# Performance work log

Hardware: AMD Instinct MI355X
Metric: run time of the kernel (lower is better)

Reference implementation:

```python
import jax, jax.numpy as jnp
import numpy as np


def setup_inputs() -> dict:
    key = jax.random.key(0)
    k1, k2, k3, k4, k5 = jax.random.split(key, 5)
    B, Di, Dh = 16384, 1024, 1024
    stdv = 1.0 / np.sqrt(Dh)
    return {
        "X": jax.random.normal(k1, (B, Di), dtype=jnp.float32),
        "h0": jax.random.normal(k2, (B, Dh), dtype=jnp.float32),
        "c0": jax.random.normal(k3, (B, Dh), dtype=jnp.float32),
        "U": jax.random.uniform(k4, (Di, 4 * Dh), dtype=jnp.float32, minval=-stdv, maxval=stdv),
        "W": jax.random.uniform(k5, (4 * Dh, Dh), dtype=jnp.float32, minval=-stdv, maxval=stdv),
    }


def reference(X, h0, c0, U, W):
    # Single-step LSTM cell: gates = X @ U + h0 @ W^T, split into i/f/g/o.
    Dh = h0.shape[-1]
    XU = X @ U                      # (B, 4*Dh)
    gates = XU + h0 @ W.T           # (B, 4*Dh)
    i, f, g, o = jnp.split(gates, 4, axis=-1)
    i = jax.nn.sigmoid(i)
    f = jax.nn.sigmoid(f)
    g = jnp.tanh(g)
    o = jax.nn.sigmoid(o)
    c = f * c0 + i * g              # (B, Dh)
    h = o * jnp.tanh(c)             # (B, Dh)
    return (h, c)
```

## Files before the change

kernel.cpp:

```cpp
#include <hip/hip_runtime.h>
#include <hip/hip_bf16.h>
#include <stdint.h>


typedef __bf16 bf16x8 __attribute__((ext_vector_type(8)));
typedef float f32x4 __attribute__((ext_vector_type(4)));

#define B_ROWS 16384
#define KDIM 2048
#define DH 1024
#define HC_ELEMS 16777216ull
#define NT 64

__device__ __forceinline__ unsigned short f2bf(float f) {
  unsigned u = __float_as_uint(f);
  u = (u + 0x7fffu + ((u >> 16) & 1u)) >> 16;
  return (unsigned short)u;
}

__device__ __forceinline__ float fsig(float x) {
  return __builtin_amdgcn_rcpf(1.0f + __expf(-x));
}
__device__ __forceinline__ float ftanh_(float x) {
  return 2.0f * __builtin_amdgcn_rcpf(1.0f + __expf(-2.0f * x)) - 1.0f;
}

__global__ void cast_concat_A(const float* __restrict__ X, const float* __restrict__ h0,
                              unsigned short* __restrict__ A) {
  size_t t = (size_t)blockIdx.x * 256 + threadIdx.x;
  size_t idx = t * 8;
  int m = (int)(idx >> 11);
  int k = (int)(idx & 2047);
  const float* src = (k < 1024) ? (X + (size_t)m * 1024 + k)
                                : (h0 + (size_t)m * 1024 + (k - 1024));
  float4 a = ((const float4*)src)[0];
  float4 b = ((const float4*)src)[1];
  union { unsigned short u[8]; uint4 v; } pk;
  pk.u[0] = f2bf(a.x); pk.u[1] = f2bf(a.y); pk.u[2] = f2bf(a.z); pk.u[3] = f2bf(a.w);
  pk.u[4] = f2bf(b.x); pk.u[5] = f2bf(b.y); pk.u[6] = f2bf(b.z); pk.u[7] = f2bf(b.w);
  *(uint4*)(A + idx) = pk.v;
}

__global__ void cast_W(const float* __restrict__ W, unsigned short* __restrict__ Bt) {
  size_t t = (size_t)blockIdx.x * 256 + threadIdx.x;
  size_t idx = t * 8;
  int n = (int)(idx >> 10);
  int k = (int)(idx & 1023);
  const float* src = W + (size_t)n * 1024 + k;
  float4 a = ((const float4*)src)[0];
  float4 b = ((const float4*)src)[1];
  union { unsigned short u[8]; uint4 v; } pk;
  pk.u[0] = f2bf(a.x); pk.u[1] = f2bf(a.y); pk.u[2] = f2bf(a.z); pk.u[3] = f2bf(a.w);
  pk.u[4] = f2bf(b.x); pk.u[5] = f2bf(b.y); pk.u[6] = f2bf(b.z); pk.u[7] = f2bf(b.w);
  *(uint4*)(Bt + (size_t)n * 2048 + 1024 + k) = pk.v;
}

__global__ void transpose_U(const float* __restrict__ U, unsigned short* __restrict__ Bt) {
  __shared__ float tile[32][33];
  int n0 = blockIdx.x * 32;
  int k0 = blockIdx.y * 32;
  int tx = threadIdx.x & 31, ty = threadIdx.x >> 5;
  #pragma unroll
  for (int i = 0; i < 4; ++i)
    tile[ty + i * 8][tx] = U[(size_t)(k0 + ty + i * 8) * 4096 + n0 + tx];
  __syncthreads();
  int nrel = threadIdx.x >> 3;
  int kc = (threadIdx.x & 7) * 4;
  union { unsigned short u[4]; uint2 v8; } pk;
  #pragma unroll
  for (int i = 0; i < 4; ++i) pk.u[i] = f2bf(tile[kc + i][nrel]);
  *(uint2*)(Bt + (size_t)(n0 + nrel) * 2048 + k0 + kc) = pk.v8;
}

__global__ __launch_bounds__(512, 2)
void lstm_gemm(const unsigned short* __restrict__ A, const unsigned short* __restrict__ Bt,
               const float* __restrict__ c0, float* __restrict__ out) {
  extern __shared__ char smem[];
  const int tid = threadIdx.x;
  const int wave = tid >> 6, lane = tid & 63;
  const int q = lane >> 4, cc = lane & 15;
  const int wm = wave >> 2, wn = wave & 3;

  const int bid = blockIdx.x;
  const int swz = (bid & 7) * 128 + (bid >> 3);
  const int m0 = (swz >> 4) * 256;
  const int j0 = (swz & 15) * 64;

  const int srow = lane >> 2;
  const int sseg = (lane & 3) ^ ((lane >> 3) & 3);
  uint32_t aoff[2], boff[2];
  #pragma unroll
  for (int u = 0; u < 2; ++u) {
    int rl = u * 128 + wave * 16 + srow;
    aoff[u] = (((uint32_t)(m0 + rl) << 11) + (uint32_t)(sseg * 8)) * 2u;
    int n = (((rl >> 4) & 3) << 10) + j0 + ((rl >> 6) << 4) + (rl & 15);
    boff[u] = (((uint32_t)n << 11) + (uint32_t)(sseg * 8)) * 2u;
  }
  const char* Ab = (const char*)A;
  const char* Bb = (const char*)Bt;

  auto stageA = [&](int tt, int slot) {
    #pragma unroll
    for (int u = 0; u < 2; ++u) {
      uintptr_t l = (uintptr_t)(smem + slot * 16384 + u * 8192 + wave * 1024);
      __builtin_amdgcn_global_load_lds(
          (const __attribute__((address_space(1))) void*)(uintptr_t)(Ab + (aoff[u] + (uint32_t)tt * 64u)),
          (__attribute__((address_space(3))) void*)(uint32_t)l, 16, 0, 0);
    }
  };
  auto stageB = [&](int tt, int slot) {
    #pragma unroll
    for (int u = 0; u < 2; ++u) {
      uintptr_t l = (uintptr_t)(smem + 65536 + slot * 16384 + u * 8192 + wave * 1024);
      __builtin_amdgcn_global_load_lds(
          (const __attribute__((address_space(1))) void*)(uintptr_t)(Bb + (boff[u] + (uint32_t)tt * 64u)),
          (__attribute__((address_space(3))) void*)(uint32_t)l, 16, 0, 0);
    }
  };

  f32x4 acc[8][4];
  #pragma unroll
  for (int a = 0; a < 8; ++a)
    #pragma unroll
    for (int b = 0; b < 4; ++b)
      acc[a][b] = f32x4{0.f, 0.f, 0.f, 0.f};

  stageA(0, 0); stageB(0, 0);
  stageA(1, 1); stageB(1, 1);
  asm volatile("s_waitcnt vmcnt(4)" ::: "memory");
  __builtin_amdgcn_s_barrier();

  const uint32_t swzq = (uint32_t)((q ^ ((cc >> 1) & 3)) * 16);
  const uint32_t aRd = (uint32_t)((wm * 128 + cc) * 64) + swzq;
  const uint32_t bRd = 65536u + (uint32_t)((wn * 64 + cc) * 64) + swzq;

  for (int t = 0; t < NT; ++t) {
    const char* sbase = smem + (t & 3) * 16384;
    const int nslot = (t + 2) & 3;
    bf16x8 af[8], bf[4];
    #pragma unroll
    for (int mi = 0; mi < 4; ++mi) af[mi] = *(const bf16x8*)(sbase + aRd + mi * 1024);
    #pragma unroll
    for (int ni = 0; ni < 4; ++ni) bf[ni] = *(const bf16x8*)(sbase + bRd + ni * 1024);
    if (t < NT - 2) stageA(t + 2, nslot);
    __builtin_amdgcn_s_barrier();
    __builtin_amdgcn_s_setprio(1);
    #pragma unroll
    for (int mi = 0; mi < 4; ++mi)
      #pragma unroll
      for (int ni = 0; ni < 4; ++ni)
        acc[mi][ni] = __builtin_amdgcn_mfma_f32_16x16x32_bf16(af[mi], bf[ni], acc[mi][ni], 0, 0, 0);
    __builtin_amdgcn_s_setprio(0);
    __builtin_amdgcn_s_barrier();
    #pragma unroll
    for (int mi = 4; mi < 8; ++mi) af[mi] = *(const bf16x8*)(sbase + aRd + mi * 1024);
    if (t < NT - 2) stageB(t + 2, nslot);
    __builtin_amdgcn_s_barrier();
    __builtin_amdgcn_s_setprio(1);
    #pragma unroll
    for (int mi = 4; mi < 8; ++mi)
      #pragma unroll
      for (int ni = 0; ni < 4; ++ni)
        acc[mi][ni] = __builtin_amdgcn_mfma_f32_16x16x32_bf16(af[mi], bf[ni], acc[mi][ni], 0, 0, 0);
    __builtin_amdgcn_s_setprio(0);
    if (t < NT - 2) asm volatile("s_waitcnt vmcnt(4)" ::: "memory");
    else            asm volatile("s_waitcnt vmcnt(0)" ::: "memory");
    __builtin_amdgcn_s_barrier();
  }

  const int gj = j0 + wn * 16 + cc;
  #pragma unroll
  for (int mi = 0; mi < 8; ++mi) {
    #pragma unroll
    for (int r = 0; r < 4; ++r) {
      int grow = m0 + wm * 128 + mi * 16 + q * 4 + r;
      float iv = fsig(acc[mi][0][r]);
      float fv = fsig(acc[mi][1][r]);
      float gv = ftanh_(acc[mi][2][r]);
      float ov = fsig(acc[mi][3][r]);
      float c0v = c0[(size_t)grow * DH + gj];
      float cv = fv * c0v + iv * gv;
      float hv = ov * ftanh_(cv);
      out[(size_t)grow * DH + gj] = hv;
      out[HC_ELEMS + (size_t)grow * DH + gj] = cv;
    }
  }
}

extern "C" void kernel_launch(void* const* d_in, const int* in_sizes, int n_in,
                              void* d_out, int out_size, void* d_ws, size_t ws_size,
                              hipStream_t stream) {
  const float* X  = (const float*)d_in[0];
  const float* h0 = (const float*)d_in[1];
  const float* c0 = (const float*)d_in[2];
  const float* U  = (const float*)d_in[3];
  const float* W  = (const float*)d_in[4];
  float* out = (float*)d_out;

  unsigned short* Abf = (unsigned short*)d_ws;
  unsigned short* Bt  = Abf + 33554432ull;

  static bool attr_set = false;
  if (!attr_set) {
    (void)hipFuncSetAttribute(reinterpret_cast<const void*>(lstm_gemm),
                              hipFuncAttributeMaxDynamicSharedMemorySize, 131072);
    attr_set = true;
  }

  cast_concat_A<<<16384, 256, 0, stream>>>(X, h0, Abf);
  cast_W<<<2048, 256, 0, stream>>>(W, Bt);
  transpose_U<<<dim3(128, 32), 256, 0, stream>>>(U, Bt);
  lstm_gemm<<<1024, 512, 131072, stream>>>(Abf, Bt, c0, out);
}
```

Before: 535.8 us.

## Use one barrier per GEMM iteration and widen cast kernels to 16 elements per thread

```diff
diff --git a/kernel.cpp b/kernel.cpp
--- a/kernel.cpp
+++ b/kernel.cpp
@@ -28,31 +28,42 @@
 __global__ void cast_concat_A(const float* __restrict__ X, const float* __restrict__ h0,
                               unsigned short* __restrict__ A) {
   size_t t = (size_t)blockIdx.x * 256 + threadIdx.x;
-  size_t idx = t * 8;
+  size_t idx = t * 16;
   int m = (int)(idx >> 11);
   int k = (int)(idx & 2047);
   const float* src = (k < 1024) ? (X + (size_t)m * 1024 + k)
                                 : (h0 + (size_t)m * 1024 + (k - 1024));
   float4 a = ((const float4*)src)[0];
   float4 b = ((const float4*)src)[1];
-  union { unsigned short u[8]; uint4 v; } pk;
+  float4 c = ((const float4*)src)[2];
+  float4 d = ((const float4*)src)[3];
+  union { unsigned short u[16]; uint4 v[2]; } pk;
   pk.u[0] = f2bf(a.x); pk.u[1] = f2bf(a.y); pk.u[2] = f2bf(a.z); pk.u[3] = f2bf(a.w);
   pk.u[4] = f2bf(b.x); pk.u[5] = f2bf(b.y); pk.u[6] = f2bf(b.z); pk.u[7] = f2bf(b.w);
-  *(uint4*)(A + idx) = pk.v;
+  pk.u[8]  = f2bf(c.x); pk.u[9]  = f2bf(c.y); pk.u[10] = f2bf(c.z); pk.u[11] = f2bf(c.w);
+  pk.u[12] = f2bf(d.x); pk.u[13] = f2bf(d.y); pk.u[14] = f2bf(d.z); pk.u[15] = f2bf(d.w);
+  *(uint4*)(A + idx) = pk.v[0];
+  *(uint4*)(A + idx + 8) = pk.v[1];
 }
 
 __global__ void cast_W(const float* __restrict__ W, unsigned short* __restrict__ Bt) {
   size_t t = (size_t)blockIdx.x * 256 + threadIdx.x;
-  size_t idx = t * 8;
+  size_t idx = t * 16;
   int n = (int)(idx >> 10);
   int k = (int)(idx & 1023);
   const float* src = W + (size_t)n * 1024 + k;
   float4 a = ((const float4*)src)[0];
   float4 b = ((const float4*)src)[1];
-  union { unsigned short u[8]; uint4 v; } pk;
+  float4 c = ((const float4*)src)[2];
+  float4 d = ((const float4*)src)[3];
+  union { unsigned short u[16]; uint4 v[2]; } pk;
   pk.u[0] = f2bf(a.x); pk.u[1] = f2bf(a.y); pk.u[2] = f2bf(a.z); pk.u[3] = f2bf(a.w);
   pk.u[4] = f2bf(b.x); pk.u[5] = f2bf(b.y); pk.u[6] = f2bf(b.z); pk.u[7] = f2bf(b.w);
-  *(uint4*)(Bt + (size_t)n * 2048 + 1024 + k) = pk.v;
+  pk.u[8]  = f2bf(c.x); pk.u[9]  = f2bf(c.y); pk.u[10] = f2bf(c.z); pk.u[11] = f2bf(c.w);
+  pk.u[12] = f2bf(d.x); pk.u[13] = f2bf(d.y); pk.u[14] = f2bf(d.z); pk.u[15] = f2bf(d.w);
+  unsigned short* dst = Bt + (size_t)n * 2048 + 1024 + k;
+  *(uint4*)(dst) = pk.v[0];
+  *(uint4*)(dst + 8) = pk.v[1];
 }
 
 __global__ void transpose_U(const float* __restrict__ U, unsigned short* __restrict__ Bt) {
@@ -136,36 +147,26 @@
 
   for (int t = 0; t < NT; ++t) {
     const char* sbase = smem + (t & 3) * 16384;
-    const int nslot = (t + 2) & 3;
+    if (t < NT - 2) {
+      const int nslot = (t + 2) & 3;
+      stageA(t + 2, nslot);
+      stageB(t + 2, nslot);
+    }
     bf16x8 af[8], bf[4];
     #pragma unroll
-    for (int mi = 0; mi < 4; ++mi) af[mi] = *(const bf16x8*)(sbase + aRd + mi * 1024);
+    for (int mi = 0; mi < 8; ++mi) af[mi] = *(const bf16x8*)(sbase + aRd + mi * 1024);
     #pragma unroll
     for (int ni = 0; ni < 4; ++ni) bf[ni] = *(const bf16x8*)(sbase + bRd + ni * 1024);
-    if (t < NT - 2) stageA(t + 2, nslot);
-    __builtin_amdgcn_s_barrier();
     __builtin_amdgcn_s_setprio(1);
     #pragma unroll
-    for (int mi = 0; mi < 4; ++mi)
+    for (int mi = 0; mi < 8; ++mi)
       #pragma unroll
       for (int ni = 0; ni < 4; ++ni)
         acc[mi][ni] = __builtin_amdgcn_mfma_f32_16x16x32_bf16(af[mi], bf[ni], acc[mi][ni], 0, 0, 0);
     __builtin_amdgcn_s_setprio(0);
-    __builtin_amdgcn_s_barrier();
-    #pragma unroll
-    for (int mi = 4; mi < 8; ++mi) af[mi] = *(const bf16x8*)(sbase + aRd + mi * 1024);
-    if (t < NT - 2) stageB(t + 2, nslot);
-    __builtin_amdgcn_s_barrier();
-    __builtin_amdgcn_s_setprio(1);
-    #pragma unroll
-    for (int mi = 4; mi < 8; ++mi)
-      #pragma unroll
-      for (int ni = 0; ni < 4; ++ni)
-        acc[mi][ni] = __builtin_amdgcn_mfma_f32_16x16x32_bf16(af[mi], bf[ni], acc[mi][ni], 0, 0, 0);
-    __builtin_amdgcn_s_setprio(0);
-    if (t < NT - 2) asm volatile("s_waitcnt vmcnt(4)" ::: "memory");
-    else            asm volatile("s_waitcnt vmcnt(0)" ::: "memory");
-    __builtin_amdgcn_s_barrier();
+    if (t < NT - 2)      asm volatile("s_waitcnt vmcnt(4)" ::: "memory");
+    else if (t == NT - 2) asm volatile("s_waitcnt vmcnt(0)" ::: "memory");
+    if (t < NT - 1) __builtin_amdgcn_s_barrier();
   }
 
   const int gj = j0 + wn * 16 + cc;
@@ -207,8 +208,8 @@
     attr_set = true;
   }
 
-  cast_concat_A<<<16384, 256, 0, stream>>>(X, h0, Abf);
-  cast_W<<<2048, 256, 0, stream>>>(W, Bt);
+  cast_concat_A<<<8192, 256, 0, stream>>>(X, h0, Abf);
+  cast_W<<<1024, 256, 0, stream>>>(W, Bt);
   transpose_U<<<dim3(128, 32), 256, 0, stream>>>(U, Bt);
   lstm_gemm<<<1024, 512, 131072, stream>>>(Abf, Bt, c0, out);
 }
```

New measurement: 529.8 us. About the same (-1.1%).
